# Performance work log

Hardware: AMD Instinct MI355X
Metric: run time of the kernel (lower is better)

## Reference

```python
import jax, jax.numpy as jnp
import numpy as np

EPS = 1e-8

def _gauss_kernel(ks=7, sigma=7.0/6.0):
    x = np.arange(ks, dtype=np.float32) - ks // 2
    g = np.exp(-0.5 * (x / sigma) ** 2)
    g = g / g.sum()
    k = np.outer(g, g).astype(np.float32)
    return jnp.asarray(k.reshape(1, 1, ks, ks))

GK = _gauss_kernel()
SOBEL_X = jnp.asarray(np.array([[1, 0, -1], [2, 0, -2], [1, 0, -1]], dtype=np.float32).reshape(1, 1, 3, 3))
SOBEL_Y = jnp.transpose(SOBEL_X, (0, 1, 3, 2))


def _conv(x, k, pad):
    return jax.lax.conv_general_dilated(
        x, k, window_strides=(1, 1), padding=[(pad, pad), (pad, pad)],
        dimension_numbers=('NCHW', 'OIHW', 'NCHW'))


def _mscn(g):
    mu = _conv(g, GK, 3)
    sigma = jnp.sqrt(jnp.abs(_conv(g * g, GK, 3) - mu * mu + EPS))
    return (g - mu) / (sigma + EPS)


def _grad_mag(g):
    gx = _conv(g, SOBEL_X, 1)
    gy = _conv(g, SOBEL_Y, 1)
    return jnp.sqrt(gx * gx + gy * gy + EPS)


def _frfsim(D, R):
    w = jnp.array([0.2989, 0.587, 0.114], dtype=D.dtype).reshape(1, 3, 1, 1)
    Dg = jnp.sum(D * w, axis=1, keepdims=True)  # (B,1,H,W)
    Rg = jnp.sum(R * w, axis=1, keepdims=True)

    # per-sample SSIM-like constants from dynamic range of Dg (calculate_C)
    d = (jnp.max(Dg, axis=(2, 3), keepdims=True) -
         jnp.min(Dg, axis=(2, 3), keepdims=True))  # (B,1,1,1)
    CM = (0.01 * d) ** 2
    CD = CM / 2.0
    CG = (0.03 * d) ** 2
    CC = CG / 2.0

    # MSCN structure map
    Dm = _mscn(Dg)
    Rm = _mscn(Rg)
    SM = (2 * Dm * Rm + CM) / (Dm ** 2 + Rm ** 2 + CM)

    # dark-channel map
    Ddc = jnp.min(D, axis=1, keepdims=True) / 255.0
    Rdc = jnp.min(R, axis=1, keepdims=True) / 255.0
    SD = (2 * Ddc * Rdc + CD) / (Ddc ** 2 + Rdc ** 2 + CD + EPS)
    mean_SD = jnp.mean(SD, axis=(1, 2, 3))  # (B,)

    # HSV color map: s = (max-min+eps)/(max+eps), v = max, color = s*v
    def color(x):
        mx = jnp.max(x, axis=1, keepdims=True)
        mn = jnp.min(x, axis=1, keepdims=True)
        return ((mx - mn + EPS) / (mx + EPS)) * mx
    Dc = color(D)
    Rc = color(R)
    SC = (2 * Dc * Rc + CC) / (Dc ** 2 + Rc ** 2 + CC + EPS)

    # Sobel gradient map
    Dgr = _grad_mag(Dg)
    Rgr = _grad_mag(Rg)
    SG = (2 * Dgr * Rgr + CG) / (Dgr ** 2 + Rgr ** 2 + CG + EPS)

    # adaptive exponents from mean dark-channel similarity
    t1 = 0.85
    b1 = jnp.where((mean_SD > t1) & (mean_SD <= 1.0), 0.2,
                   jnp.where((mean_SD >= 0.0) & (mean_SD <= t1), 0.8, 0.5))
    b2 = jnp.where((mean_SD > t1) & (mean_SD <= 1.0), 0.8,
                   jnp.where((mean_SD >= 0.0) & (mean_SD <= t1), 0.2, 0.5))
    b1 = b1.astype(D.dtype).reshape(-1, 1, 1, 1)
    b2 = b2.astype(D.dtype).reshape(-1, 1, 1, 1)

    # safe_pow(base, b) == |base|^b (complex pow of |base|+0j, real part)
    frfsimmap = jnp.power(jnp.abs(SM * SD), b1) * jnp.power(SG * SC, b2)
    frfsimval = jnp.mean(jnp.abs(frfsimmap), axis=(1, 2, 3))  # (B,)
    return jnp.mean(frfsimval)  # == sum_i frfsimval_i / B


def setup_inputs() -> dict:
    key = jax.random.key(0)
    kD, kR = jax.random.split(key)
    B, H, W = 32, 512, 512
    D = jax.random.uniform(kD, (B, 3, H, W), dtype=jnp.float32)
    R = jax.random.uniform(kR, (B, 3, H, W), dtype=jnp.float32)
    return {"D": D, "R": R}


def reference(D, R):
    return _frfsim(D, R)
```

## Files before the change

kernel.cpp:

```cpp
#include <hip/hip_runtime.h>

#define EPSF  1e-8f
#define IMG_W 512
#define IMG_H 512
#define HWPX  (IMG_W*IMG_H)
#define NB    32


__global__ void k_init(unsigned* __restrict__ minb, unsigned* __restrict__ maxb,
                       float* __restrict__ sdsum, float* __restrict__ cand) {
  int t = threadIdx.x;
  if (t < NB) { minb[t] = 0x7F7FFFFFu;  maxb[t] = 0u; sdsum[t] = 0.f; }
  if (t < 3*NB) cand[t] = 0.f;
}

__global__ __launch_bounds__(256) void k_minmax(const float* __restrict__ D,
                                                unsigned* __restrict__ minb,
                                                unsigned* __restrict__ maxb) {
  const int b = blockIdx.y, chunk = blockIdx.x, tid = threadIdx.x;
  const float4* P0 = (const float4*)(D + (size_t)b * 3 * HWPX);
  const float4* P1 = P0 + HWPX/4;
  const float4* P2 = P1 + HWPX/4;
  float mn = __uint_as_float(0x7F7FFFFFu), mx = 0.f;
  const int base = chunk * 2048;
  #pragma unroll
  for (int it = 0; it < 8; ++it) {
    int i = base + it*256 + tid;
    float4 a = P0[i], c = P1[i], e = P2[i];
    float g;
    g = 0.2989f*a.x + 0.587f*c.x + 0.114f*e.x; mn = fminf(mn,g); mx = fmaxf(mx,g);
    g = 0.2989f*a.y + 0.587f*c.y + 0.114f*e.y; mn = fminf(mn,g); mx = fmaxf(mx,g);
    g = 0.2989f*a.z + 0.587f*c.z + 0.114f*e.z; mn = fminf(mn,g); mx = fmaxf(mx,g);
    g = 0.2989f*a.w + 0.587f*c.w + 0.114f*e.w; mn = fminf(mn,g); mx = fmaxf(mx,g);
  }
  #pragma unroll
  for (int o = 32; o > 0; o >>= 1) {
    mn = fminf(mn, __shfl_down(mn, o, 64));
    mx = fmaxf(mx, __shfl_down(mx, o, 64));
  }
  __shared__ float smn[4], smx[4];
  if ((tid & 63) == 0) { smn[tid>>6] = mn; smx[tid>>6] = mx; }
  __syncthreads();
  if (tid == 0) {
    mn = fminf(fminf(smn[0],smn[1]), fminf(smn[2],smn[3]));
    mx = fmaxf(fmaxf(smx[0],smx[1]), fmaxf(smx[2],smx[3]));
    atomicMin(minb + b, __float_as_uint(mn));
    atomicMax(maxb + b, __float_as_uint(mx));
  }
}

#define TW 64
#define TH 32
#define HALO 3
#define SW (TW+2*HALO)
#define SH (TH+2*HALO)

__global__ __launch_bounds__(256) void k_main(const float* __restrict__ D, const float* __restrict__ R,
                                              const unsigned* __restrict__ minb,
                                              const unsigned* __restrict__ maxb,
                                              float* __restrict__ sdsum,
                                              float* __restrict__ cand) {
  __shared__ float sDg[SH][SW];
  __shared__ float sRg[SH][SW];
  __shared__ float sSD[TH][TW];
  __shared__ float sSC[TH][TW];

  const int tid = threadIdx.x;
  const int b   = blockIdx.z;
  const int tx0 = blockIdx.x * TW;
  const int ty0 = blockIdx.y * TH;

  const float dr = __uint_as_float(maxb[b]) - __uint_as_float(minb[b]);
  const float CM = (0.01f*dr)*(0.01f*dr);
  const float CD = 0.5f*CM;
  const float CG = (0.03f*dr)*(0.03f*dr);
  const float CC = 0.5f*CG;

  const float* D0 = D + (size_t)b*3*HWPX;
  const float* D1 = D0 + HWPX;
  const float* D2 = D1 + HWPX;
  const float* R0 = R + (size_t)b*3*HWPX;
  const float* R1 = R0 + HWPX;
  const float* R2 = R1 + HWPX;

  float sdacc = 0.f;

  for (int i = tid; i < SH*SW; i += 256) {
    int r = i / SW, c = i % SW;
    int gy = ty0 - HALO + r, gx = tx0 - HALO + c;
    float dg = 0.f, rg = 0.f;
    if ((unsigned)gy < IMG_H && (unsigned)gx < IMG_W) {
      size_t off = (size_t)gy*IMG_W + gx;
      float d0=D0[off], d1=D1[off], d2=D2[off];
      float r0=R0[off], r1=R1[off], r2=R2[off];
      dg = 0.2989f*d0 + 0.587f*d1 + 0.114f*d2;
      rg = 0.2989f*r0 + 0.587f*r1 + 0.114f*r2;
      if (r >= HALO && r < HALO+TH && c >= HALO && c < HALO+TW) {
        float dmn = fminf(fminf(d0,d1),d2);
        float rmn = fminf(fminf(r0,r1),r2);
        float a_ = dmn*(1.f/255.f), c_ = rmn*(1.f/255.f);
        float sd = (2.f*a_*c_ + CD)/(a_*a_ + c_*c_ + CD + EPSF);
        sSD[r-HALO][c-HALO] = sd;
        sdacc += sd;
        float dmx = fmaxf(fmaxf(d0,d1),d2);
        float rmx = fmaxf(fmaxf(r0,r1),r2);
        float dcol = ((dmx-dmn+EPSF)/(dmx+EPSF))*dmx;
        float rcol = ((rmx-rmn+EPSF)/(rmx+EPSF))*rmx;
        sSC[r-HALO][c-HALO] = (2.f*dcol*rcol + CC)/(dcol*dcol + rcol*rcol + CC + EPSF);
      }
    }
    sDg[r][c] = dg;
    sRg[r][c] = rg;
  }
  __syncthreads();

  float gw[7];
  {
    float sum = 0.f;
    #pragma unroll
    for (int j = 0; j < 7; ++j) {
      float t = (float)(j-3) * (6.f/7.f);
      float v = expf(-0.5f * t * t);
      gw[j] = v; sum += v;
    }
    float inv = 1.f/sum;
    #pragma unroll
    for (int j = 0; j < 7; ++j) gw[j] *= inv;
  }

  const int x   = tid & 63;
  const int yo0 = (tid >> 6) * 8;

  float whgD[7], whqD[7], whgR[7], whqR[7];
  float wsxD[7], wsyD[7], wsxR[7], wsyR[7];
  float a0 = 0.f, a1 = 0.f, a2 = 0.f;

  #pragma unroll
  for (int step = 0; step < 14; ++step) {
    const int r = yo0 + step;
    float vD[7], vR[7];
    #pragma unroll
    for (int j = 0; j < 7; ++j) { vD[j] = sDg[r][x+j]; vR[j] = sRg[r][x+j]; }
    float hgD=0.f, hqD=0.f, hgR=0.f, hqR=0.f;
    #pragma unroll
    for (int j = 0; j < 7; ++j) {
      hgD += gw[j]*vD[j]; hqD += gw[j]*vD[j]*vD[j];
      hgR += gw[j]*vR[j]; hqR += gw[j]*vR[j]*vR[j];
    }
    float sxD = vD[2]-vD[4], syD = vD[2]+2.f*vD[3]+vD[4];
    float sxR = vR[2]-vR[4], syR = vR[2]+2.f*vR[3]+vR[4];
    #pragma unroll
    for (int j = 0; j < 6; ++j) {
      whgD[j]=whgD[j+1]; whqD[j]=whqD[j+1]; whgR[j]=whgR[j+1]; whqR[j]=whqR[j+1];
      wsxD[j]=wsxD[j+1]; wsyD[j]=wsyD[j+1]; wsxR[j]=wsxR[j+1]; wsyR[j]=wsyR[j+1];
    }
    whgD[6]=hgD; whqD[6]=hqD; whgR[6]=hgR; whqR[6]=hqR;
    wsxD[6]=sxD; wsyD[6]=syD; wsxR[6]=sxR; wsyR[6]=syR;

    if (step >= 6) {
      const int yo = yo0 + step - 6;
      float muD=0.f, exD=0.f, muR=0.f, exR=0.f;
      #pragma unroll
      for (int j = 0; j < 7; ++j) {
        muD += gw[j]*whgD[j]; exD += gw[j]*whqD[j];
        muR += gw[j]*whgR[j]; exR += gw[j]*whqR[j];
      }
      float v0D = sDg[yo+HALO][x+HALO];
      float v0R = sRg[yo+HALO][x+HALO];
      float sigD = sqrtf(fabsf(exD - muD*muD + EPSF));
      float sigR = sqrtf(fabsf(exR - muR*muR + EPSF));
      float Dm = (v0D - muD) / (sigD + EPSF);
      float Rm = (v0R - muR) / (sigR + EPSF);
      float SM = (2.f*Dm*Rm + CM) / (Dm*Dm + Rm*Rm + CM);
      float gxD = wsxD[2] + 2.f*wsxD[3] + wsxD[4];
      float gyD = wsyD[2] - wsyD[4];
      float gxR = wsxR[2] + 2.f*wsxR[3] + wsxR[4];
      float gyR = wsyR[2] - wsyR[4];
      float GD = sqrtf(gxD*gxD + gyD*gyD + EPSF);
      float GR = sqrtf(gxR*gxR + gyR*gyR + EPSF);
      float SG = (2.f*GD*GR + CG) / (GD*GD + GR*GR + CG + EPSF);
      float SDv = sSD[yo][x];
      float SCv = sSC[yo][x];
      float m1 = fabsf(SM * SDv);
      float m2 = SG * SCv;
      float l1 = log2f(m1);
      float l2 = log2f(m2);
      a0 += exp2f(0.2f*l1 + 0.8f*l2);
      a1 += exp2f(0.8f*l1 + 0.2f*l2);
      a2 += exp2f(0.5f*l1 + 0.5f*l2);
    }
  }

  #pragma unroll
  for (int o = 32; o > 0; o >>= 1) {
    sdacc += __shfl_down(sdacc, o, 64);
    a0    += __shfl_down(a0,    o, 64);
    a1    += __shfl_down(a1,    o, 64);
    a2    += __shfl_down(a2,    o, 64);
  }
  __shared__ float red[4][4];
  const int w = tid >> 6;
  if ((tid & 63) == 0) { red[w][0]=sdacc; red[w][1]=a0; red[w][2]=a1; red[w][3]=a2; }
  __syncthreads();
  if (tid < 4) {
    float t = red[0][tid]+red[1][tid]+red[2][tid]+red[3][tid];
    if (tid == 0) atomicAdd(sdsum + b, t);
    else          atomicAdd(cand + (tid-1)*NB + b, t);
  }
}

__global__ void k_final(const float* __restrict__ sdsum, const float* __restrict__ cand,
                        float* __restrict__ out) {
  const int t = threadIdx.x;
  float v = 0.f;
  if (t < NB) {
    float meanSD = sdsum[t] * (1.f/(float)HWPX);
    float c;
    if      (meanSD > 0.85f && meanSD <= 1.0f)  c = cand[0*NB + t];
    else if (meanSD >= 0.f  && meanSD <= 0.85f) c = cand[1*NB + t];
    else                                        c = cand[2*NB + t];
    v = c;
  }
  #pragma unroll
  for (int o = 32; o > 0; o >>= 1) v += __shfl_down(v, o, 64);
  if (t == 0) out[0] = v * (1.f/8388608.f);
}

extern "C" void kernel_launch(void* const* d_in, const int* in_sizes, int n_in,
                              void* d_out, int out_size, void* d_ws, size_t ws_size,
                              hipStream_t stream) {
  (void)in_sizes; (void)n_in; (void)out_size; (void)ws_size;
  const float* D = (const float*)d_in[0];
  const float* R = (const float*)d_in[1];
  float* out = (float*)d_out;
  unsigned* minb  = (unsigned*)d_ws;
  unsigned* maxb  = minb + NB;
  float*    sdsum = (float*)(maxb + NB);
  float*    cand  = sdsum + NB;

  k_init  <<<1, 128, 0, stream>>>(minb, maxb, sdsum, cand);
  k_minmax<<<dim3(32, NB), 256, 0, stream>>>(D, minb, maxb);
  k_main  <<<dim3(IMG_W/TW, IMG_H/TH, NB), 256, 0, stream>>>(D, R, minb, maxb, sdsum, cand);
  k_final <<<1, 64, 0, stream>>>(sdsum, cand, out);
}
```

Measured before the change: 333.8 us.

## Vectorize tile loads, use fast math intrinsics, symmetric Gaussian weights, wider minmax grid

The main kernel's halo load now reads float4 chunks over a padded 72-wide shared tile, computing grayscale and the dark-channel and color maps four pixels at a time. Precise division, sqrt, log and exp are replaced by AMD hardware approximations (rcp, sqrt, log, exp2). The Gaussian weights become folded symmetric constants, the Sobel window shrinks to five entries, and launch bounds request four blocks per CU. The minmax kernel uses four times more blocks with less work each to raise parallelism. The approximate intrinsics trade some accuracy for fewer instructions, and the wider halo loads some extra data.

New measurement: 635.0 us. +90.2%, slower.

```diff
diff --git a/kernel.cpp b/kernel.cpp
--- a/kernel.cpp
+++ b/kernel.cpp
@@ -6,11 +6,21 @@
 #define HWPX  (IMG_W*IMG_H)
 #define NB    32
 
+#define GW0 0.0125602730f
+#define GW1 0.0788280293f
+#define GW2 0.2372963577f
+#define GW3 0.3426321149f
+
+#define RCPF(x)  __builtin_amdgcn_rcpf(x)
+#define SQRTF(x) __builtin_amdgcn_sqrtf(x)
+#define LOG2F(x) __builtin_amdgcn_logf(x)
+#define EXP2F(x) __builtin_amdgcn_exp2f(x)
+
 
 __global__ void k_init(unsigned* __restrict__ minb, unsigned* __restrict__ maxb,
                        float* __restrict__ sdsum, float* __restrict__ cand) {
   int t = threadIdx.x;
-  if (t < NB) { minb[t] = 0x7F7FFFFFu;  maxb[t] = 0u; sdsum[t] = 0.f; }
+  if (t < NB) { minb[t] = 0x7F7FFFFFu; maxb[t] = 0u; sdsum[t] = 0.f; }
   if (t < 3*NB) cand[t] = 0.f;
 }
 
@@ -21,18 +31,20 @@
   const float4* P0 = (const float4*)(D + (size_t)b * 3 * HWPX);
   const float4* P1 = P0 + HWPX/4;
   const float4* P2 = P1 + HWPX/4;
+  const int i0 = chunk * 512 + tid;
+  const int i1 = i0 + 256;
+  float4 a0 = P0[i0], c0 = P1[i0], e0 = P2[i0];
+  float4 a1 = P0[i1], c1 = P1[i1], e1 = P2[i1];
   float mn = __uint_as_float(0x7F7FFFFFu), mx = 0.f;
-  const int base = chunk * 2048;
-  #pragma unroll
-  for (int it = 0; it < 8; ++it) {
-    int i = base + it*256 + tid;
-    float4 a = P0[i], c = P1[i], e = P2[i];
-    float g;
-    g = 0.2989f*a.x + 0.587f*c.x + 0.114f*e.x; mn = fminf(mn,g); mx = fmaxf(mx,g);
-    g = 0.2989f*a.y + 0.587f*c.y + 0.114f*e.y; mn = fminf(mn,g); mx = fmaxf(mx,g);
-    g = 0.2989f*a.z + 0.587f*c.z + 0.114f*e.z; mn = fminf(mn,g); mx = fmaxf(mx,g);
-    g = 0.2989f*a.w + 0.587f*c.w + 0.114f*e.w; mn = fminf(mn,g); mx = fmaxf(mx,g);
-  }
+  float g;
+  g = 0.2989f*a0.x + 0.587f*c0.x + 0.114f*e0.x; mn = fminf(mn,g); mx = fmaxf(mx,g);
+  g = 0.2989f*a0.y + 0.587f*c0.y + 0.114f*e0.y; mn = fminf(mn,g); mx = fmaxf(mx,g);
+  g = 0.2989f*a0.z + 0.587f*c0.z + 0.114f*e0.z; mn = fminf(mn,g); mx = fmaxf(mx,g);
+  g = 0.2989f*a0.w + 0.587f*c0.w + 0.114f*e0.w; mn = fminf(mn,g); mx = fmaxf(mx,g);
+  g = 0.2989f*a1.x + 0.587f*c1.x + 0.114f*e1.x; mn = fminf(mn,g); mx = fmaxf(mx,g);
+  g = 0.2989f*a1.y + 0.587f*c1.y + 0.114f*e1.y; mn = fminf(mn,g); mx = fmaxf(mx,g);
+  g = 0.2989f*a1.z + 0.587f*c1.z + 0.114f*e1.z; mn = fminf(mn,g); mx = fmaxf(mx,g);
+  g = 0.2989f*a1.w + 0.587f*c1.w + 0.114f*e1.w; mn = fminf(mn,g); mx = fmaxf(mx,g);
   #pragma unroll
   for (int o = 32; o > 0; o >>= 1) {
     mn = fminf(mn, __shfl_down(mn, o, 64));
@@ -52,16 +64,17 @@
 #define TW 64
 #define TH 32
 #define HALO 3
-#define SW (TW+2*HALO)
-#define SH (TH+2*HALO)
-
-__global__ __launch_bounds__(256) void k_main(const float* __restrict__ D, const float* __restrict__ R,
-                                              const unsigned* __restrict__ minb,
-                                              const unsigned* __restrict__ maxb,
-                                              float* __restrict__ sdsum,
-                                              float* __restrict__ cand) {
-  __shared__ float sDg[SH][SW];
-  __shared__ float sRg[SH][SW];
+#define SWP 72
+#define SH  38
+#define NCHUNK (SH*18)
+
+__global__ __launch_bounds__(256, 4) void k_main(const float* __restrict__ D, const float* __restrict__ R,
+                                                 const unsigned* __restrict__ minb,
+                                                 const unsigned* __restrict__ maxb,
+                                                 float* __restrict__ sdsum,
+                                                 float* __restrict__ cand) {
+  __shared__ float sDg[SH][SWP];
+  __shared__ float sRg[SH][SWP];
   __shared__ float sSD[TH][TW];
   __shared__ float sSC[TH][TW];
 
@@ -77,62 +90,65 @@
   const float CC = 0.5f*CG;
 
   const float* D0 = D + (size_t)b*3*HWPX;
-  const float* D1 = D0 + HWPX;
-  const float* D2 = D1 + HWPX;
   const float* R0 = R + (size_t)b*3*HWPX;
-  const float* R1 = R0 + HWPX;
-  const float* R2 = R1 + HWPX;
+  const float4* fD0 = (const float4*)D0;
+  const float4* fD1 = fD0 + HWPX/4;
+  const float4* fD2 = fD1 + HWPX/4;
+  const float4* fR0 = (const float4*)R0;
+  const float4* fR1 = fR0 + HWPX/4;
+  const float4* fR2 = fR1 + HWPX/4;
 
   float sdacc = 0.f;
 
-  for (int i = tid; i < SH*SW; i += 256) {
-    int r = i / SW, c = i % SW;
-    int gy = ty0 - HALO + r, gx = tx0 - HALO + c;
-    float dg = 0.f, rg = 0.f;
-    if ((unsigned)gy < IMG_H && (unsigned)gx < IMG_W) {
-      size_t off = (size_t)gy*IMG_W + gx;
-      float d0=D0[off], d1=D1[off], d2=D2[off];
-      float r0=R0[off], r1=R1[off], r2=R2[off];
-      dg = 0.2989f*d0 + 0.587f*d1 + 0.114f*d2;
-      rg = 0.2989f*r0 + 0.587f*r1 + 0.114f*r2;
-      if (r >= HALO && r < HALO+TH && c >= HALO && c < HALO+TW) {
-        float dmn = fminf(fminf(d0,d1),d2);
-        float rmn = fminf(fminf(r0,r1),r2);
-        float a_ = dmn*(1.f/255.f), c_ = rmn*(1.f/255.f);
-        float sd = (2.f*a_*c_ + CD)/(a_*a_ + c_*c_ + CD + EPSF);
-        sSD[r-HALO][c-HALO] = sd;
-        sdacc += sd;
-        float dmx = fmaxf(fmaxf(d0,d1),d2);
-        float rmx = fmaxf(fmaxf(r0,r1),r2);
-        float dcol = ((dmx-dmn+EPSF)/(dmx+EPSF))*dmx;
-        float rcol = ((rmx-rmn+EPSF)/(rmx+EPSF))*rmx;
-        sSC[r-HALO][c-HALO] = (2.f*dcol*rcol + CC)/(dcol*dcol + rcol*rcol + CC + EPSF);
+  const int cx0 = tx0 - 4;
+  for (int j = tid; j < NCHUNK; j += 256) {
+    const int r  = j / 18;
+    const int c  = j - r*18;
+    const int gy = ty0 - HALO + r;
+    const int gx = cx0 + c*4;
+    float4 dg4 = make_float4(0.f,0.f,0.f,0.f);
+    float4 rg4 = make_float4(0.f,0.f,0.f,0.f);
+    if ((unsigned)gy < IMG_H && gx >= 0 && gx < IMG_W) {
+      const int o4 = gy*(IMG_W/4) + (gx >> 2);
+      float4 d0 = fD0[o4], d1 = fD1[o4], d2 = fD2[o4];
+      float4 r0 = fR0[o4], r1 = fR1[o4], r2 = fR2[o4];
+      dg4.x = 0.2989f*d0.x + 0.587f*d1.x + 0.114f*d2.x;
+      dg4.y = 0.2989f*d0.y + 0.587f*d1.y + 0.114f*d2.y;
+      dg4.z = 0.2989f*d0.z + 0.587f*d1.z + 0.114f*d2.z;
+      dg4.w = 0.2989f*d0.w + 0.587f*d1.w + 0.114f*d2.w;
+      rg4.x = 0.2989f*r0.x + 0.587f*r1.x + 0.114f*r2.x;
+      rg4.y = 0.2989f*r0.y + 0.587f*r1.y + 0.114f*r2.y;
+      rg4.z = 0.2989f*r0.z + 0.587f*r1.z + 0.114f*r2.z;
+      rg4.w = 0.2989f*r0.w + 0.587f*r1.w + 0.114f*r2.w;
+      if (r >= HALO && r < HALO+TH && c >= 1 && c <= 16) {
+        float4 sd4, sc4;
+        #define MAPS(f) { \
+          float dmn = fminf(fminf(d0.f,d1.f),d2.f); \
+          float rmn = fminf(fminf(r0.f,r1.f),r2.f); \
+          float a_ = dmn*(1.f/255.f), c_ = rmn*(1.f/255.f); \
+          float sd = (2.f*a_*c_ + CD) * RCPF(a_*a_ + c_*c_ + CD + EPSF); \
+          sd4.f = sd; sdacc += sd; \
+          float dmx = fmaxf(fmaxf(d0.f,d1.f),d2.f); \
+          float rmx = fmaxf(fmaxf(r0.f,r1.f),r2.f); \
+          float dcol = ((dmx-dmn+EPSF) * RCPF(dmx+EPSF)) * dmx; \
+          float rcol = ((rmx-rmn+EPSF) * RCPF(rmx+EPSF)) * rmx; \
+          sc4.f = (2.f*dcol*rcol + CC) * RCPF(dcol*dcol + rcol*rcol + CC + EPSF); }
+        MAPS(x) MAPS(y) MAPS(z) MAPS(w)
+        #undef MAPS
+        *(float4*)&sSD[r-HALO][(c-1)*4] = sd4;
+        *(float4*)&sSC[r-HALO][(c-1)*4] = sc4;
       }
     }
-    sDg[r][c] = dg;
-    sRg[r][c] = rg;
+    *(float4*)&sDg[r][c*4] = dg4;
+    *(float4*)&sRg[r][c*4] = rg4;
   }
   __syncthreads();
-
-  float gw[7];
-  {
-    float sum = 0.f;
-    #pragma unroll
-    for (int j = 0; j < 7; ++j) {
-      float t = (float)(j-3) * (6.f/7.f);
-      float v = expf(-0.5f * t * t);
-      gw[j] = v; sum += v;
-    }
-    float inv = 1.f/sum;
-    #pragma unroll
-    for (int j = 0; j < 7; ++j) gw[j] *= inv;
-  }
 
   const int x   = tid & 63;
   const int yo0 = (tid >> 6) * 8;
 
-  float whgD[7], whqD[7], whgR[7], whqR[7];
-  float wsxD[7], wsyD[7], wsxR[7], wsyR[7];
+  float whgD[7]={0}, whqD[7]={0}, whgR[7]={0}, whqR[7]={0};
+  float wsxD[5]={0}, wsyD[5]={0}, wsxR[5]={0}, wsyR[5]={0};
   float a0 = 0.f, a1 = 0.f, a2 = 0.f;
 
   #pragma unroll
@@ -140,54 +156,57 @@
     const int r = yo0 + step;
     float vD[7], vR[7];
     #pragma unroll
-    for (int j = 0; j < 7; ++j) { vD[j] = sDg[r][x+j]; vR[j] = sRg[r][x+j]; }
-    float hgD=0.f, hqD=0.f, hgR=0.f, hqR=0.f;
-    #pragma unroll
-    for (int j = 0; j < 7; ++j) {
-      hgD += gw[j]*vD[j]; hqD += gw[j]*vD[j]*vD[j];
-      hgR += gw[j]*vR[j]; hqR += gw[j]*vR[j]*vR[j];
-    }
+    for (int j = 0; j < 7; ++j) { vD[j] = sDg[r][x+1+j]; vR[j] = sRg[r][x+1+j]; }
+    float hgD, hqD, hgR, hqR;
+    hgD = GW0*(vD[0]+vD[6]) + GW1*(vD[1]+vD[5]) + GW2*(vD[2]+vD[4]) + GW3*vD[3];
+    hgR = GW0*(vR[0]+vR[6]) + GW1*(vR[1]+vR[5]) + GW2*(vR[2]+vR[4]) + GW3*vR[3];
+    hqD = GW0*(vD[0]*vD[0]+vD[6]*vD[6]) + GW1*(vD[1]*vD[1]+vD[5]*vD[5])
+        + GW2*(vD[2]*vD[2]+vD[4]*vD[4]) + GW3*vD[3]*vD[3];
+    hqR = GW0*(vR[0]*vR[0]+vR[6]*vR[6]) + GW1*(vR[1]*vR[1]+vR[5]*vR[5])
+        + GW2*(vR[2]*vR[2]+vR[4]*vR[4]) + GW3*vR[3]*vR[3];
     float sxD = vD[2]-vD[4], syD = vD[2]+2.f*vD[3]+vD[4];
     float sxR = vR[2]-vR[4], syR = vR[2]+2.f*vR[3]+vR[4];
     #pragma unroll
     for (int j = 0; j < 6; ++j) {
       whgD[j]=whgD[j+1]; whqD[j]=whqD[j+1]; whgR[j]=whgR[j+1]; whqR[j]=whqR[j+1];
+    }
+    whgD[6]=hgD; whqD[6]=hqD; whgR[6]=hgR; whqR[6]=hqR;
+    #pragma unroll
+    for (int j = 0; j < 4; ++j) {
       wsxD[j]=wsxD[j+1]; wsyD[j]=wsyD[j+1]; wsxR[j]=wsxR[j+1]; wsyR[j]=wsyR[j+1];
     }
-    whgD[6]=hgD; whqD[6]=hqD; whgR[6]=hgR; whqR[6]=hqR;
-    wsxD[6]=sxD; wsyD[6]=syD; wsxR[6]=sxR; wsyR[6]=syR;
+    wsxD[4]=sxD; wsyD[4]=syD; wsxR[4]=sxR; wsyR[4]=syR;
 
     if (step >= 6) {
       const int yo = yo0 + step - 6;
-      float muD=0.f, exD=0.f, muR=0.f, exR=0.f;
-      #pragma unroll
-      for (int j = 0; j < 7; ++j) {
-        muD += gw[j]*whgD[j]; exD += gw[j]*whqD[j];
-        muR += gw[j]*whgR[j]; exR += gw[j]*whqR[j];
-      }
-      float v0D = sDg[yo+HALO][x+HALO];
-      float v0R = sRg[yo+HALO][x+HALO];
-      float sigD = sqrtf(fabsf(exD - muD*muD + EPSF));
-      float sigR = sqrtf(fabsf(exR - muR*muR + EPSF));
-      float Dm = (v0D - muD) / (sigD + EPSF);
-      float Rm = (v0R - muR) / (sigR + EPSF);
-      float SM = (2.f*Dm*Rm + CM) / (Dm*Dm + Rm*Rm + CM);
-      float gxD = wsxD[2] + 2.f*wsxD[3] + wsxD[4];
-      float gyD = wsyD[2] - wsyD[4];
-      float gxR = wsxR[2] + 2.f*wsxR[3] + wsxR[4];
-      float gyR = wsyR[2] - wsyR[4];
-      float GD = sqrtf(gxD*gxD + gyD*gyD + EPSF);
-      float GR = sqrtf(gxR*gxR + gyR*gyR + EPSF);
-      float SG = (2.f*GD*GR + CG) / (GD*GD + GR*GR + CG + EPSF);
+      float muD, exD, muR, exR;
+      muD = GW0*(whgD[0]+whgD[6]) + GW1*(whgD[1]+whgD[5]) + GW2*(whgD[2]+whgD[4]) + GW3*whgD[3];
+      exD = GW0*(whqD[0]+whqD[6]) + GW1*(whqD[1]+whqD[5]) + GW2*(whqD[2]+whqD[4]) + GW3*whqD[3];
+      muR = GW0*(whgR[0]+whgR[6]) + GW1*(whgR[1]+whgR[5]) + GW2*(whgR[2]+whgR[4]) + GW3*whgR[3];
+      exR = GW0*(whqR[0]+whqR[6]) + GW1*(whqR[1]+whqR[5]) + GW2*(whqR[2]+whqR[4]) + GW3*whqR[3];
+      float v0D = sDg[yo+HALO][x+4];
+      float v0R = sRg[yo+HALO][x+4];
+      float sigD = SQRTF(fabsf(exD - muD*muD + EPSF));
+      float sigR = SQRTF(fabsf(exR - muR*muR + EPSF));
+      float Dm = (v0D - muD) * RCPF(sigD + EPSF);
+      float Rm = (v0R - muR) * RCPF(sigR + EPSF);
+      float SM = (2.f*Dm*Rm + CM) * RCPF(Dm*Dm + Rm*Rm + CM);
+      float gxD = wsxD[0] + 2.f*wsxD[1] + wsxD[2];
+      float gyD = wsyD[0] - wsyD[2];
+      float gxR = wsxR[0] + 2.f*wsxR[1] + wsxR[2];
+      float gyR = wsyR[0] - wsyR[2];
+      float GD = SQRTF(gxD*gxD + gyD*gyD + EPSF);
+      float GR = SQRTF(gxR*gxR + gyR*gyR + EPSF);
+      float SG = (2.f*GD*GR + CG) * RCPF(GD*GD + GR*GR + CG + EPSF);
       float SDv = sSD[yo][x];
       float SCv = sSC[yo][x];
       float m1 = fabsf(SM * SDv);
       float m2 = SG * SCv;
-      float l1 = log2f(m1);
-      float l2 = log2f(m2);
-      a0 += exp2f(0.2f*l1 + 0.8f*l2);
-      a1 += exp2f(0.8f*l1 + 0.2f*l2);
-      a2 += exp2f(0.5f*l1 + 0.5f*l2);
+      float l1 = LOG2F(m1);
+      float l2 = LOG2F(m2);
+      a0 += EXP2F(0.2f*l1 + 0.8f*l2);
+      a1 += EXP2F(0.8f*l1 + 0.2f*l2);
+      a2 += EXP2F(0.5f*l1 + 0.5f*l2);
     }
   }
 
@@ -239,7 +258,7 @@
   float*    cand  = sdsum + NB;
 
   k_init  <<<1, 128, 0, stream>>>(minb, maxb, sdsum, cand);
-  k_minmax<<<dim3(32, NB), 256, 0, stream>>>(D, minb, maxb);
+  k_minmax<<<dim3(128, NB), 256, 0, stream>>>(D, minb, maxb);
   k_main  <<<dim3(IMG_W/TW, IMG_H/TH, NB), 256, 0, stream>>>(D, R, minb, maxb, sdsum, cand);
   k_final <<<1, 64, 0, stream>>>(sdsum, cand, out);
 }
```
